# Optimization experiments

Measured on AMD Instinct MI355X. Metric: run time of the kernel, lower is better.

## Reference

```python
import jax, jax.numpy as jnp
import numpy as np

N1, N2, D = 8192, 8192, 128

def setup_inputs() -> dict:
    key = jax.random.key(0)
    k1, k2, k3, k4 = jax.random.split(key, 4)
    X1 = jax.random.normal(k1, (N1, D), dtype=jnp.float32)
    X2 = jax.random.normal(k2, (N2, D), dtype=jnp.float32)
    task1 = jax.random.randint(k3, (N1,), 0, 2, dtype=jnp.int32)
    task2 = jax.random.randint(k4, (N2,), 0, 2, dtype=jnp.int32)
    # learned parameters (init values match module defaults: lengthscale=1, output_variance=1, b=0)
    log_l = jnp.zeros((D,), dtype=jnp.float32)          # log(1)
    log_theta_l = jnp.zeros((1,), dtype=jnp.float32)    # log(1)
    b = jnp.zeros((1,), dtype=jnp.float32)
    return {"X1": X1, "X2": X2, "log_l": log_l, "log_theta_l": log_theta_l,
            "b": b, "task1": task1, "task2": task2}

def reference(X1, X2, log_l, log_theta_l, b, task1, task2):
    l = jnp.exp(log_l)                      # (D,) ARD lengthscales
    A = X1 / l                              # (N1, D)
    B = X2 / l                              # (N2, D)
    # sum((a-b)^2) = |a|^2 + |b|^2 - 2 a.b  -> GEMM form, no (N1,N2,D) intermediate
    sq_dist = (jnp.sum(A * A, axis=1)[:, None]
               + jnp.sum(B * B, axis=1)[None, :]
               - 2.0 * (A @ B.T))
    sq_dist = jnp.maximum(sq_dist, 0.0)
    K_base = jnp.exp(log_theta_l[0]) * jnp.exp(-0.5 * sq_dist)   # (N1, N2)
    # lambda = clip(2/(1+exp(b)) - 1, 0, 1)
    lam = jnp.clip(2.0 / (1.0 + jnp.exp(b[0])) - 1.0, 0.0, 1.0)
    diff_task = task1[:, None] != task2[None, :]                 # (N1, N2) bool
    K = K_base * jnp.where(diff_task, lam, 1.0)
    return K
```

## Files before the change

kernel.cpp:

```cpp
#include <hip/hip_runtime.h>
#include <stdint.h>

typedef float f32x4 __attribute__((ext_vector_type(4)));
typedef int   i32x4 __attribute__((ext_vector_type(4)));
typedef __bf16 bf16x8 __attribute__((ext_vector_type(8)));

#define NN 8192
#define DDIM 128

#define APRIME_OFF 0u
#define BPRIME_OFF (8192u*512u)
#define NORM_OFF   (268435456u - 65536u)

__device__ __forceinline__ uint32_t pk2(__bf16 a, __bf16 b) {
    return (uint32_t)__builtin_bit_cast(unsigned short, a)
         | ((uint32_t)__builtin_bit_cast(unsigned short, b) << 16);
}

__device__ __forceinline__ void gload_lds16(const void* g, void* l) {
    __builtin_amdgcn_global_load_lds(
        (const __attribute__((address_space(1))) uint32_t*)g,
        (__attribute__((address_space(3))) uint32_t*)l,
        16, 0, 0);
}

__global__ __launch_bounds__(256) void prep_kernel(
    const float* __restrict__ X1, const float* __restrict__ X2,
    const float* __restrict__ log_l, char* __restrict__ outbuf)
{
    int t = threadIdx.x, wave = t >> 6, lane = t & 63;
    int row = blockIdx.x * 4 + wave;
    const float* X; uint32_t base; float* nrm;
    if (row < NN) {
        X = X1 + (size_t)row * DDIM;
        base = APRIME_OFF + (uint32_t)row * 512u;
        nrm = (float*)(outbuf + NORM_OFF) + row;
    } else {
        int r2 = row - NN;
        X = X2 + (size_t)r2 * DDIM;
        base = BPRIME_OFF + (uint32_t)r2 * 512u;
        nrm = (float*)(outbuf + NORM_OFF) + NN + r2;
    }
    int c0 = lane * 2;
    float2 x = *(const float2*)(X + c0);
    float a0 = x.x * __expf(-log_l[c0]);
    float a1 = x.y * __expf(-log_l[c0 + 1]);
    float ss = a0 * a0 + a1 * a1;
    #pragma unroll
    for (int o = 32; o; o >>= 1) ss += __shfl_down(ss, o);
    if (lane == 0) *nrm = ss;
    __bf16 h0 = (__bf16)a0, h1 = (__bf16)a1;
    __bf16 l0 = (__bf16)(a0 - (float)h0), l1 = (__bf16)(a1 - (float)h1);
    int m = lane >> 2;
    int c = m >> 2;
    int sh = m & 3;
    int sl = 4 | sh;
    int rs = row & 7;
    uint32_t offh = base + (uint32_t)c * 128u + (uint32_t)((sh ^ rs) * 16) + (uint32_t)(lane & 3) * 4u;
    uint32_t offl = base + (uint32_t)c * 128u + (uint32_t)((sl ^ rs) * 16) + (uint32_t)(lane & 3) * 4u;
    *(uint32_t*)(outbuf + offh) = pk2(h0, h1);
    *(uint32_t*)(outbuf + offl) = pk2(l0, l1);
}

__global__ __launch_bounds__(256, 3) void fast_kernel(
    const char* __restrict__ stash,
    const int* __restrict__ task1, const int* __restrict__ task2,
    const float* __restrict__ log_theta_l, const float* __restrict__ bparam,
    float* __restrict__ C)
{
    __shared__ __align__(16) char smem[32768];
    const int t = threadIdx.x;
    const int lane = t & 63, wv = t >> 6;
    const int wr = wv >> 1, wc = wv & 1;
    const int lr = lane & 15, lg = lane >> 4;

    int wg = blockIdx.x;
    int swz = (wg & 7) * 488 + (wg >> 3);
    int tm = 2 + (swz >> 6);
    int tn = swz & 63;

    const char* Abase = stash + APRIME_OFF + (size_t)tm * 128 * 512;
    const char* Bbase = stash + BPRIME_OFF + (size_t)tn * 128 * 512;

    f32x4 acc[4][4];
    #pragma unroll
    for (int i = 0; i < 4; ++i)
        #pragma unroll
        for (int j = 0; j < 4; ++j) acc[i][j] = (f32x4){0.f, 0.f, 0.f, 0.f};

    #define STAGE(c) do {                                                         \
        _Pragma("unroll")                                                         \
        for (int i = 0; i < 4; ++i) {                                             \
            int l = t + i * 256;                                                  \
            gload_lds16(Abase + (size_t)(l >> 3) * 512 + (c) * 128 + (l & 7) * 16,\
                        smem + l * 16);                                           \
            gload_lds16(Bbase + (size_t)(l >> 3) * 512 + (c) * 128 + (l & 7) * 16,\
                        smem + 16384 + l * 16);                                   \
        }                                                                         \
    } while (0)

    #define FRAGMM() do {                                                         \
        bf16x8 ah[4], bh[4], xf[4];                                               \
        _Pragma("unroll")                                                         \
        for (int mi = 0; mi < 4; ++mi) {                                          \
            int row = wr * 64 + mi * 16 + lr;                                     \
            ah[mi] = *(const bf16x8*)(smem + row * 128 + ((lg ^ (row & 7)) * 16));\
        }                                                                         \
        _Pragma("unroll")                                                         \
        for (int ni = 0; ni < 4; ++ni) {                                          \
            int row = wc * 64 + ni * 16 + lr;                                     \
            bh[ni] = *(const bf16x8*)(smem + 16384 + row * 128                    \
                      + ((lg ^ (row & 7)) * 16));                                 \
        }                                                                         \
        _Pragma("unroll")                                                         \
        for (int mi = 0; mi < 4; ++mi)                                            \
            _Pragma("unroll")                                                     \
            for (int ni = 0; ni < 4; ++ni)                                        \
                acc[mi][ni] = __builtin_amdgcn_mfma_f32_16x16x32_bf16(            \
                    bh[ni], ah[mi], acc[mi][ni], 0, 0, 0);                        \
        _Pragma("unroll")                                                         \
        for (int mi = 0; mi < 4; ++mi) {                                          \
            int row = wr * 64 + mi * 16 + lr;                                     \
            xf[mi] = *(const bf16x8*)(smem + row * 128                            \
                      + (((4 | lg) ^ (row & 7)) * 16));                           \
        }                                                                         \
        _Pragma("unroll")                                                         \
        for (int mi = 0; mi < 4; ++mi)                                            \
            _Pragma("unroll")                                                     \
            for (int ni = 0; ni < 4; ++ni)                                        \
                acc[mi][ni] = __builtin_amdgcn_mfma_f32_16x16x32_bf16(            \
                    bh[ni], xf[mi], acc[mi][ni], 0, 0, 0);                        \
        _Pragma("unroll")                                                         \
        for (int ni = 0; ni < 4; ++ni) {                                          \
            int row = wc * 64 + ni * 16 + lr;                                     \
            xf[ni] = *(const bf16x8*)(smem + 16384 + row * 128                    \
                      + (((4 | lg) ^ (row & 7)) * 16));                           \
        }                                                                         \
        _Pragma("unroll")                                                         \
        for (int mi = 0; mi < 4; ++mi)                                            \
            _Pragma("unroll")                                                     \
            for (int ni = 0; ni < 4; ++ni)                                        \
                acc[mi][ni] = __builtin_amdgcn_mfma_f32_16x16x32_bf16(            \
                    xf[ni], ah[mi], acc[mi][ni], 0, 0, 0);                        \
    } while (0)

    STAGE(0);
    __syncthreads();
    FRAGMM();
    #pragma unroll
    for (int c = 1; c < 4; ++c) {
        __syncthreads();
        STAGE(c);
        __syncthreads();
        FRAGMM();
    }

    const float* n1g = (const float*)(stash + NORM_OFF);
    const float* n2g = n1g + NN;
    float logt = log_theta_l[0];
    float bb = bparam[0];
    float lam = fminf(fmaxf(2.f / (1.f + __expf(bb)) - 1.f, 0.f), 1.f);
    int rbase = tm * 128, cbase = tn * 128;

    #pragma unroll
    for (int mi = 0; mi < 4; ++mi) {
        int rowl = wr * 64 + mi * 16 + lr;
        float n1v = n1g[rbase + rowl];
        int t1v = task1[rbase + rowl];
        #pragma unroll
        for (int ni = 0; ni < 4; ++ni) {
            int coll = wc * 64 + ni * 16 + lg * 4;
            f32x4 n2v = *(const f32x4*)(n2g + cbase + coll);
            i32x4 t2v = *(const i32x4*)(task2 + cbase + coll);
            f32x4 kv;
            #pragma unroll
            for (int rix = 0; rix < 4; ++rix) {
                float s = fmaxf(n1v + n2v[rix] - 2.f * acc[mi][ni][rix], 0.f);
                float k = __expf(fmaf(-0.5f, s, logt));
                kv[rix] = (t1v != t2v[rix]) ? k * lam : k;
            }
            *(f32x4*)(C + (size_t)(rbase + rowl) * NN + cbase + coll) = kv;
        }
    }
    #undef STAGE
    #undef FRAGMM
}

#define RSTRIDE 80
#define S_AH 0
#define S_AL 10240
#define S_BH 20480
#define S_BL 30720
#define S_ILS 40960
#define S_N1  41472
#define S_N2  41984
#define S_TOT 42496

__device__ __forceinline__ void split4(f32x4 x, uint2& hi, uint2& lo) {
    __bf16 h0 = (__bf16)x[0], h1 = (__bf16)x[1], h2 = (__bf16)x[2], h3 = (__bf16)x[3];
    hi.x = pk2(h0, h1); hi.y = pk2(h2, h3);
    __bf16 l0 = (__bf16)(x[0] - (float)h0);
    __bf16 l1 = (__bf16)(x[1] - (float)h1);
    __bf16 l2 = (__bf16)(x[2] - (float)h2);
    __bf16 l3 = (__bf16)(x[3] - (float)h3);
    lo.x = pk2(l0, l1); lo.y = pk2(l2, l3);
}

__device__ __forceinline__ void lds_barrier() {
    asm volatile("s_waitcnt lgkmcnt(0)" ::: "memory");
    __builtin_amdgcn_sched_barrier(0);
    __builtin_amdgcn_s_barrier();
    __builtin_amdgcn_sched_barrier(0);
}

__global__ __launch_bounds__(256, 3) void slow_kernel(
    const float* __restrict__ X1, const float* __restrict__ X2,
    const float* __restrict__ log_l,
    const float* __restrict__ log_theta_l, const float* __restrict__ bparam,
    const int* __restrict__ task1, const int* __restrict__ task2,
    float* __restrict__ C)
{
    __shared__ __align__(16) char smem[S_TOT];
    float* const ils = (float*)(smem + S_ILS);
    float* const n1s = (float*)(smem + S_N1);
    float* const n2s = (float*)(smem + S_N2);

    const int t = threadIdx.x;
    const int lane = t & 63;
    const int wv = t >> 6;
    const int wr = wv >> 1, wc = wv & 1;
    const int lr = lane & 15, lg = lane >> 4;
    const int kq = t & 7;
    const int rg = t >> 3;

    int wg = blockIdx.x;
    int tsel = wg >> 6;
    int tm = (tsel == 2) ? 63 : tsel;
    int tn = wg & 63;

    const float* Ag = X1 + (size_t)tm * 128 * DDIM;
    const float* Bg = X2 + (size_t)tn * 128 * DDIM;

    if (t < 128) ils[t] = __expf(-log_l[t]);

    f32x4 aV[4], bV[4];
    #pragma unroll
    for (int e = 0; e < 4; ++e) {
        aV[e] = *(const f32x4*)(Ag + (size_t)(e * 32 + rg) * DDIM + kq * 4);
        bV[e] = *(const f32x4*)(Bg + (size_t)(e * 32 + rg) * DDIM + kq * 4);
    }
    __syncthreads();

    float nA[4] = {0.f, 0.f, 0.f, 0.f};
    float nB[4] = {0.f, 0.f, 0.f, 0.f};
    f32x4 acc[4][4];
    #pragma unroll
    for (int i = 0; i < 4; ++i)
        #pragma unroll
        for (int j = 0; j < 4; ++j) acc[i][j] = (f32x4){0.f, 0.f, 0.f, 0.f};

    for (int c = 0; c < 4; ++c) {
        {
            f32x4 il4 = *(const f32x4*)(ils + c * 32 + kq * 4);
            #pragma unroll
            for (int e = 0; e < 4; ++e) {
                int rr = e * 32 + rg;
                f32x4 xa = aV[e] * il4;
                f32x4 xb = bV[e] * il4;
                nA[e] += xa[0]*xa[0] + xa[1]*xa[1] + xa[2]*xa[2] + xa[3]*xa[3];
                nB[e] += xb[0]*xb[0] + xb[1]*xb[1] + xb[2]*xb[2] + xb[3]*xb[3];
                uint2 hA, lA, hB, lB;
                split4(xa, hA, lA);
                split4(xb, hB, lB);
                int boff = rr * RSTRIDE + kq * 8;
                *(uint2*)(smem + S_AH + boff) = hA;
                *(uint2*)(smem + S_AL + boff) = lA;
                *(uint2*)(smem + S_BH + boff) = hB;
                *(uint2*)(smem + S_BL + boff) = lB;
            }
        }
        if (c < 3) {
            #pragma unroll
            for (int e = 0; e < 4; ++e) {
                aV[e] = *(const f32x4*)(Ag + (size_t)(e * 32 + rg) * DDIM + (c + 1) * 32 + kq * 4);
                bV[e] = *(const f32x4*)(Bg + (size_t)(e * 32 + rg) * DDIM + (c + 1) * 32 + kq * 4);
            }
        }
        lds_barrier();
        {
            bf16x8 ah[4], bh[4], xf[4];
            #pragma unroll
            for (int mi = 0; mi < 4; ++mi) {
                int off = (wr * 64 + mi * 16 + lr) * RSTRIDE + lg * 16;
                ah[mi] = *(const bf16x8*)(smem + S_AH + off);
            }
            #pragma unroll
            for (int ni = 0; ni < 4; ++ni) {
                int off = (wc * 64 + ni * 16 + lr) * RSTRIDE + lg * 16;
                bh[ni] = *(const bf16x8*)(smem + S_BH + off);
            }
            #pragma unroll
            for (int mi = 0; mi < 4; ++mi)
                #pragma unroll
                for (int ni = 0; ni < 4; ++ni)
                    acc[mi][ni] = __builtin_amdgcn_mfma_f32_16x16x32_bf16(bh[ni], ah[mi], acc[mi][ni], 0, 0, 0);
            #pragma unroll
            for (int mi = 0; mi < 4; ++mi) {
                int off = (wr * 64 + mi * 16 + lr) * RSTRIDE + lg * 16;
                xf[mi] = *(const bf16x8*)(smem + S_AL + off);
            }
            #pragma unroll
            for (int mi = 0; mi < 4; ++mi)
                #pragma unroll
                for (int ni = 0; ni < 4; ++ni)
                    acc[mi][ni] = __builtin_amdgcn_mfma_f32_16x16x32_bf16(bh[ni], xf[mi], acc[mi][ni], 0, 0, 0);
            #pragma unroll
            for (int ni = 0; ni < 4; ++ni) {
                int off = (wc * 64 + ni * 16 + lr) * RSTRIDE + lg * 16;
                xf[ni] = *(const bf16x8*)(smem + S_BL + off);
            }
            #pragma unroll
            for (int mi = 0; mi < 4; ++mi)
                #pragma unroll
                for (int ni = 0; ni < 4; ++ni)
                    acc[mi][ni] = __builtin_amdgcn_mfma_f32_16x16x32_bf16(xf[ni], ah[mi], acc[mi][ni], 0, 0, 0);
        }
        lds_barrier();
    }

    #pragma unroll
    for (int e = 0; e < 4; ++e) {
        #pragma unroll
        for (int off = 1; off < 8; off <<= 1) {
            nA[e] += __shfl_xor(nA[e], off);
            nB[e] += __shfl_xor(nB[e], off);
        }
    }
    if (kq == 0) {
        #pragma unroll
        for (int e = 0; e < 4; ++e) {
            n1s[e * 32 + rg] = nA[e];
            n2s[e * 32 + rg] = nB[e];
        }
    }
    __syncthreads();

    float logt = log_theta_l[0];
    float bb = bparam[0];
    float lam = fminf(fmaxf(2.f / (1.f + __expf(bb)) - 1.f, 0.f), 1.f);
    int rbase = tm * 128, cbase = tn * 128;

    #pragma unroll
    for (int mi = 0; mi < 4; ++mi) {
        int rowl = wr * 64 + mi * 16 + lr;
        float n1v = n1s[rowl];
        int t1v = task1[rbase + rowl];
        #pragma unroll
        for (int ni = 0; ni < 4; ++ni) {
            int coll = wc * 64 + ni * 16 + lg * 4;
            f32x4 n2v = *(const f32x4*)(n2s + coll);
            i32x4 t2v = *(const i32x4*)(task2 + cbase + coll);
            f32x4 kv;
            #pragma unroll
            for (int rix = 0; rix < 4; ++rix) {
                float s = fmaxf(n1v + n2v[rix] - 2.f * acc[mi][ni][rix], 0.f);
                float k = __expf(fmaf(-0.5f, s, logt));
                kv[rix] = (t1v != t2v[rix]) ? k * lam : k;
            }
            *(f32x4*)(C + (size_t)(rbase + rowl) * NN + cbase + coll) = kv;
        }
    }
}

extern "C" void kernel_launch(void* const* d_in, const int* in_sizes, int n_in,
                              void* d_out, int out_size, void* d_ws, size_t ws_size,
                              hipStream_t stream)
{
    const float* X1 = (const float*)d_in[0];
    const float* X2 = (const float*)d_in[1];
    const float* log_l = (const float*)d_in[2];
    const float* log_theta = (const float*)d_in[3];
    const float* bp = (const float*)d_in[4];
    const int* t1 = (const int*)d_in[5];
    const int* t2 = (const int*)d_in[6];
    float* C = (float*)d_out;
    (void)d_ws; (void)ws_size; (void)in_sizes; (void)n_in; (void)out_size;

    prep_kernel<<<4096, 256, 0, stream>>>(X1, X2, log_l, (char*)d_out);
    fast_kernel<<<3904, 256, 0, stream>>>((const char*)d_out, t1, t2, log_theta, bp, C);
    slow_kernel<<<192, 256, 0, stream>>>(X1, X2, log_l, log_theta, bp, t1, t2, C);
}
```

Baseline: 101.0 us.

## Split tail tile rows and slow-kernel tiles into 64x64 quarter blocks

The fast kernel now handles tile row 62 as 256 quarter-sized 64x64 blocks instead of full 128x128 tiles, and the slow kernel (rows 0, 1, 63, whose stash region overlaps the output) is split into 768 quarter-tile blocks instead of 192 full tiles. The goal is better load balance and more parallelism in the tail of each launch, so the small slow kernel is not bound by a handful of long-running workgroups. In exchange, the quarter tiles reuse less data per load and pay more per-block overhead.

```diff
diff --git a/kernel.cpp b/kernel.cpp
--- a/kernel.cpp
+++ b/kernel.cpp
@@ -71,130 +71,235 @@
     __shared__ __align__(16) char smem[32768];
     const int t = threadIdx.x;
     const int lane = t & 63, wv = t >> 6;
-    const int wr = wv >> 1, wc = wv & 1;
     const int lr = lane & 15, lg = lane >> 4;
-
-    int wg = blockIdx.x;
-    int swz = (wg & 7) * 488 + (wg >> 3);
-    int tm = 2 + (swz >> 6);
-    int tn = swz & 63;
-
-    const char* Abase = stash + APRIME_OFF + (size_t)tm * 128 * 512;
-    const char* Bbase = stash + BPRIME_OFF + (size_t)tn * 128 * 512;
-
-    f32x4 acc[4][4];
-    #pragma unroll
-    for (int i = 0; i < 4; ++i)
-        #pragma unroll
-        for (int j = 0; j < 4; ++j) acc[i][j] = (f32x4){0.f, 0.f, 0.f, 0.f};
-
-    #define STAGE(c) do {                                                         \
-        _Pragma("unroll")                                                         \
-        for (int i = 0; i < 4; ++i) {                                             \
-            int l = t + i * 256;                                                  \
-            gload_lds16(Abase + (size_t)(l >> 3) * 512 + (c) * 128 + (l & 7) * 16,\
-                        smem + l * 16);                                           \
-            gload_lds16(Bbase + (size_t)(l >> 3) * 512 + (c) * 128 + (l & 7) * 16,\
-                        smem + 16384 + l * 16);                                   \
-        }                                                                         \
-    } while (0)
-
-    #define FRAGMM() do {                                                         \
-        bf16x8 ah[4], bh[4], xf[4];                                               \
-        _Pragma("unroll")                                                         \
-        for (int mi = 0; mi < 4; ++mi) {                                          \
-            int row = wr * 64 + mi * 16 + lr;                                     \
-            ah[mi] = *(const bf16x8*)(smem + row * 128 + ((lg ^ (row & 7)) * 16));\
-        }                                                                         \
-        _Pragma("unroll")                                                         \
-        for (int ni = 0; ni < 4; ++ni) {                                          \
-            int row = wc * 64 + ni * 16 + lr;                                     \
-            bh[ni] = *(const bf16x8*)(smem + 16384 + row * 128                    \
-                      + ((lg ^ (row & 7)) * 16));                                 \
-        }                                                                         \
-        _Pragma("unroll")                                                         \
-        for (int mi = 0; mi < 4; ++mi)                                            \
-            _Pragma("unroll")                                                     \
-            for (int ni = 0; ni < 4; ++ni)                                        \
-                acc[mi][ni] = __builtin_amdgcn_mfma_f32_16x16x32_bf16(            \
-                    bh[ni], ah[mi], acc[mi][ni], 0, 0, 0);                        \
-        _Pragma("unroll")                                                         \
-        for (int mi = 0; mi < 4; ++mi) {                                          \
-            int row = wr * 64 + mi * 16 + lr;                                     \
-            xf[mi] = *(const bf16x8*)(smem + row * 128                            \
-                      + (((4 | lg) ^ (row & 7)) * 16));                           \
-        }                                                                         \
-        _Pragma("unroll")                                                         \
-        for (int mi = 0; mi < 4; ++mi)                                            \
-            _Pragma("unroll")                                                     \
-            for (int ni = 0; ni < 4; ++ni)                                        \
-                acc[mi][ni] = __builtin_amdgcn_mfma_f32_16x16x32_bf16(            \
-                    bh[ni], xf[mi], acc[mi][ni], 0, 0, 0);                        \
-        _Pragma("unroll")                                                         \
-        for (int ni = 0; ni < 4; ++ni) {                                          \
-            int row = wc * 64 + ni * 16 + lr;                                     \
-            xf[ni] = *(const bf16x8*)(smem + 16384 + row * 128                    \
-                      + (((4 | lg) ^ (row & 7)) * 16));                           \
-        }                                                                         \
-        _Pragma("unroll")                                                         \
-        for (int mi = 0; mi < 4; ++mi)                                            \
-            _Pragma("unroll")                                                     \
-            for (int ni = 0; ni < 4; ++ni)                                        \
-                acc[mi][ni] = __builtin_amdgcn_mfma_f32_16x16x32_bf16(            \
-                    xf[ni], ah[mi], acc[mi][ni], 0, 0, 0);                        \
-    } while (0)
-
-    STAGE(0);
-    __syncthreads();
-    FRAGMM();
-    #pragma unroll
-    for (int c = 1; c < 4; ++c) {
-        __syncthreads();
-        STAGE(c);
-        __syncthreads();
-        FRAGMM();
-    }
-
     const float* n1g = (const float*)(stash + NORM_OFF);
     const float* n2g = n1g + NN;
     float logt = log_theta_l[0];
     float bb = bparam[0];
     float lam = fminf(fmaxf(2.f / (1.f + __expf(bb)) - 1.f, 0.f), 1.f);
-    int rbase = tm * 128, cbase = tn * 128;
-
-    #pragma unroll
-    for (int mi = 0; mi < 4; ++mi) {
-        int rowl = wr * 64 + mi * 16 + lr;
-        float n1v = n1g[rbase + rowl];
-        int t1v = task1[rbase + rowl];
-        #pragma unroll
-        for (int ni = 0; ni < 4; ++ni) {
-            int coll = wc * 64 + ni * 16 + lg * 4;
-            f32x4 n2v = *(const f32x4*)(n2g + cbase + coll);
-            i32x4 t2v = *(const i32x4*)(task2 + cbase + coll);
-            f32x4 kv;
-            #pragma unroll
-            for (int rix = 0; rix < 4; ++rix) {
-                float s = fmaxf(n1v + n2v[rix] - 2.f * acc[mi][ni][rix], 0.f);
-                float k = __expf(fmaf(-0.5f, s, logt));
-                kv[rix] = (t1v != t2v[rix]) ? k * lam : k;
-            }
-            *(f32x4*)(C + (size_t)(rbase + rowl) * NN + cbase + coll) = kv;
-        }
-    }
-    #undef STAGE
-    #undef FRAGMM
+    int wg = blockIdx.x;
+
+    if (wg < 3840) {
+        const int wr = wv >> 1, wc = wv & 1;
+        int swz = (wg & 7) * 480 + (wg >> 3);
+        int tm = 2 + (swz >> 6);
+        int tn = swz & 63;
+        const char* Abase = stash + APRIME_OFF + (size_t)tm * 128 * 512;
+        const char* Bbase = stash + BPRIME_OFF + (size_t)tn * 128 * 512;
+
+        f32x4 acc[4][4];
+        #pragma unroll
+        for (int i = 0; i < 4; ++i)
+            #pragma unroll
+            for (int j = 0; j < 4; ++j) acc[i][j] = (f32x4){0.f, 0.f, 0.f, 0.f};
+
+        #define STAGE_F(c) do {                                                       \
+            _Pragma("unroll")                                                         \
+            for (int i = 0; i < 4; ++i) {                                             \
+                int l = t + i * 256;                                                  \
+                gload_lds16(Abase + (size_t)(l >> 3) * 512 + (c) * 128 + (l & 7) * 16,\
+                            smem + l * 16);                                           \
+                gload_lds16(Bbase + (size_t)(l >> 3) * 512 + (c) * 128 + (l & 7) * 16,\
+                            smem + 16384 + l * 16);                                   \
+            }                                                                         \
+        } while (0)
+
+        #define FRAGMM_F() do {                                                       \
+            bf16x8 ah[4], bh[4], xf[4];                                               \
+            _Pragma("unroll")                                                         \
+            for (int mi = 0; mi < 4; ++mi) {                                          \
+                int row = wr * 64 + mi * 16 + lr;                                     \
+                ah[mi] = *(const bf16x8*)(smem + row * 128 + ((lg ^ (row & 7)) * 16));\
+            }                                                                         \
+            _Pragma("unroll")                                                         \
+            for (int ni = 0; ni < 4; ++ni) {                                          \
+                int row = wc * 64 + ni * 16 + lr;                                     \
+                bh[ni] = *(const bf16x8*)(smem + 16384 + row * 128                    \
+                          + ((lg ^ (row & 7)) * 16));                                 \
+            }                                                                         \
+            _Pragma("unroll")                                                         \
+            for (int mi = 0; mi < 4; ++mi)                                            \
+                _Pragma("unroll")                                                     \
+                for (int ni = 0; ni < 4; ++ni)                                        \
+                    acc[mi][ni] = __builtin_amdgcn_mfma_f32_16x16x32_bf16(            \
+                        bh[ni], ah[mi], acc[mi][ni], 0, 0, 0);                        \
+            _Pragma("unroll")                                                         \
+            for (int mi = 0; mi < 4; ++mi) {                                          \
+                int row = wr * 64 + mi * 16 + lr;                                     \
+                xf[mi] = *(const bf16x8*)(smem + row * 128                            \
+                          + (((4 | lg) ^ (row & 7)) * 16));                           \
+            }                                                                         \
+            _Pragma("unroll")                                                         \
+            for (int mi = 0; mi < 4; ++mi)                                            \
+                _Pragma("unroll")                                                     \
+                for (int ni = 0; ni < 4; ++ni)                                        \
+                    acc[mi][ni] = __builtin_amdgcn_mfma_f32_16x16x32_bf16(            \
+                        bh[ni], xf[mi], acc[mi][ni], 0, 0, 0);                        \
+            _Pragma("unroll")                                                         \
+            for (int ni = 0; ni < 4; ++ni) {                                          \
+                int row = wc * 64 + ni * 16 + lr;                                     \
+                xf[ni] = *(const bf16x8*)(smem + 16384 + row * 128                    \
+                          + (((4 | lg) ^ (row & 7)) * 16));                           \
+            }                                                                         \
+            _Pragma("unroll")                                                         \
+            for (int mi = 0; mi < 4; ++mi)                                            \
+                _Pragma("unroll")                                                     \
+                for (int ni = 0; ni < 4; ++ni)                                        \
+                    acc[mi][ni] = __builtin_amdgcn_mfma_f32_16x16x32_bf16(            \
+                        xf[ni], ah[mi], acc[mi][ni], 0, 0, 0);                        \
+        } while (0)
+
+        STAGE_F(0);
+        __syncthreads();
+        FRAGMM_F();
+        #pragma unroll
+        for (int c = 1; c < 4; ++c) {
+            __syncthreads();
+            STAGE_F(c);
+            __syncthreads();
+            FRAGMM_F();
+        }
+
+        int rbase = tm * 128, cbase = tn * 128;
+        #pragma unroll
+        for (int mi = 0; mi < 4; ++mi) {
+            int rowl = wr * 64 + mi * 16 + lr;
+            float n1v = n1g[rbase + rowl];
+            int t1v = task1[rbase + rowl];
+            #pragma unroll
+            for (int ni = 0; ni < 4; ++ni) {
+                int coll = wc * 64 + ni * 16 + lg * 4;
+                f32x4 n2v = *(const f32x4*)(n2g + cbase + coll);
+                i32x4 t2v = *(const i32x4*)(task2 + cbase + coll);
+                f32x4 kv;
+                #pragma unroll
+                for (int rix = 0; rix < 4; ++rix) {
+                    float s = fmaxf(n1v + n2v[rix] - 2.f * acc[mi][ni][rix], 0.f);
+                    float k = __expf(fmaf(-0.5f, s, logt));
+                    kv[rix] = (t1v != t2v[rix]) ? k * lam : k;
+                }
+                *(f32x4*)(C + (size_t)(rbase + rowl) * NN + cbase + coll) = kv;
+            }
+        }
+        #undef STAGE_F
+        #undef FRAGMM_F
+    } else {
+        int wq = wg - 3840;
+        int tn = wq >> 2;
+        int q = wq & 3;
+        int arow0 = 62 * 128 + (q >> 1) * 64;
+        int brow0 = tn * 128 + (q & 1) * 64;
+        const int wr = wv >> 1, wc = wv & 1;
+        const char* Abase = stash + APRIME_OFF + (size_t)arow0 * 512;
+        const char* Bbase = stash + BPRIME_OFF + (size_t)brow0 * 512;
+
+        f32x4 acc[2][2];
+        #pragma unroll
+        for (int i = 0; i < 2; ++i)
+            #pragma unroll
+            for (int j = 0; j < 2; ++j) acc[i][j] = (f32x4){0.f, 0.f, 0.f, 0.f};
+
+        #define STAGE_Q(c) do {                                                       \
+            _Pragma("unroll")                                                         \
+            for (int i = 0; i < 2; ++i) {                                             \
+                int l = t + i * 256;                                                  \
+                gload_lds16(Abase + (size_t)(l >> 3) * 512 + (c) * 128 + (l & 7) * 16,\
+                            smem + l * 16);                                           \
+                gload_lds16(Bbase + (size_t)(l >> 3) * 512 + (c) * 128 + (l & 7) * 16,\
+                            smem + 8192 + l * 16);                                    \
+            }                                                                         \
+        } while (0)
+
+        #define FRAGMM_Q() do {                                                       \
+            bf16x8 ah[2], bh[2], xf[2];                                               \
+            _Pragma("unroll")                                                         \
+            for (int mi = 0; mi < 2; ++mi) {                                          \
+                int row = wr * 32 + mi * 16 + lr;                                     \
+                ah[mi] = *(const bf16x8*)(smem + row * 128 + ((lg ^ (row & 7)) * 16));\
+            }                                                                         \
+            _Pragma("unroll")                                                         \
+            for (int ni = 0; ni < 2; ++ni) {                                          \
+                int row = wc * 32 + ni * 16 + lr;                                     \
+                bh[ni] = *(const bf16x8*)(smem + 8192 + row * 128                     \
+                          + ((lg ^ (row & 7)) * 16));                                 \
+            }                                                                         \
+            _Pragma("unroll")                                                         \
+            for (int mi = 0; mi < 2; ++mi)                                            \
+                _Pragma("unroll")                                                     \
+                for (int ni = 0; ni < 2; ++ni)                                        \
+                    acc[mi][ni] = __builtin_amdgcn_mfma_f32_16x16x32_bf16(            \
+                        bh[ni], ah[mi], acc[mi][ni], 0, 0, 0);                        \
+            _Pragma("unroll")                                                         \
+            for (int mi = 0; mi < 2; ++mi) {                                          \
+                int row = wr * 32 + mi * 16 + lr;                                     \
+                xf[mi] = *(const bf16x8*)(smem + row * 128                            \
+                          + (((4 | lg) ^ (row & 7)) * 16));                           \
+            }                                                                         \
+            _Pragma("unroll")                                                         \
+            for (int mi = 0; mi < 2; ++mi)                                            \
+                _Pragma("unroll")                                                     \
+                for (int ni = 0; ni < 2; ++ni)                                        \
+                    acc[mi][ni] = __builtin_amdgcn_mfma_f32_16x16x32_bf16(            \
+                        bh[ni], xf[mi], acc[mi][ni], 0, 0, 0);                        \
+            _Pragma("unroll")                                                         \
+            for (int ni = 0; ni < 2; ++ni) {                                          \
+                int row = wc * 32 + ni * 16 + lr;                                     \
+                xf[ni] = *(const bf16x8*)(smem + 8192 + row * 128                     \
+                          + (((4 | lg) ^ (row & 7)) * 16));                           \
+            }                                                                         \
+            _Pragma("unroll")                                                         \
+            for (int mi = 0; mi < 2; ++mi)                                            \
+                _Pragma("unroll")                                                     \
+                for (int ni = 0; ni < 2; ++ni)                                        \
+                    acc[mi][ni] = __builtin_amdgcn_mfma_f32_16x16x32_bf16(            \
+                        xf[ni], ah[mi], acc[mi][ni], 0, 0, 0);                        \
+        } while (0)
+
+        STAGE_Q(0);
+        __syncthreads();
+        FRAGMM_Q();
+        #pragma unroll
+        for (int c = 1; c < 4; ++c) {
+            __syncthreads();
+            STAGE_Q(c);
+            __syncthreads();
+            FRAGMM_Q();
+        }
+
+        #pragma unroll
+        for (int mi = 0; mi < 2; ++mi) {
+            int rowl = wr * 32 + mi * 16 + lr;
+            float n1v = n1g[arow0 + rowl];
+            int t1v = task1[arow0 + rowl];
+            #pragma unroll
+            for (int ni = 0; ni < 2; ++ni) {
+                int coll = wc * 32 + ni * 16 + lg * 4;
+                f32x4 n2v = *(const f32x4*)(n2g + brow0 + coll);
+                i32x4 t2v = *(const i32x4*)(task2 + brow0 + coll);
+                f32x4 kv;
+                #pragma unroll
+                for (int rix = 0; rix < 4; ++rix) {
+                    float s = fmaxf(n1v + n2v[rix] - 2.f * acc[mi][ni][rix], 0.f);
+                    float k = __expf(fmaf(-0.5f, s, logt));
+                    kv[rix] = (t1v != t2v[rix]) ? k * lam : k;
+                }
+                *(f32x4*)(C + (size_t)(arow0 + rowl) * NN + brow0 + coll) = kv;
+            }
+        }
+        #undef STAGE_Q
+        #undef FRAGMM_Q
+    }
 }
 
 #define RSTRIDE 80
-#define S_AH 0
-#define S_AL 10240
-#define S_BH 20480
-#define S_BL 30720
-#define S_ILS 40960
-#define S_N1  41472
-#define S_N2  41984
-#define S_TOT 42496
+#define SQ_AH 0
+#define SQ_AL 5120
+#define SQ_BH 10240
+#define SQ_BL 15360
+#define SQ_ILS 20480
+#define SQ_N1  20992
+#define SQ_N2  21504
+#define SQ_TOT 22016
 
 __device__ __forceinline__ void split4(f32x4 x, uint2& hi, uint2& lo) {
     __bf16 h0 = (__bf16)x[0], h1 = (__bf16)x[1], h2 = (__bf16)x[2], h3 = (__bf16)x[3];
@@ -220,10 +325,10 @@
     const int* __restrict__ task1, const int* __restrict__ task2,
     float* __restrict__ C)
 {
-    __shared__ __align__(16) char smem[S_TOT];
-    float* const ils = (float*)(smem + S_ILS);
-    float* const n1s = (float*)(smem + S_N1);
-    float* const n2s = (float*)(smem + S_N2);
+    __shared__ __align__(16) char smem[SQ_TOT];
+    float* const ils = (float*)(smem + SQ_ILS);
+    float* const n1s = (float*)(smem + SQ_N1);
+    float* const n2s = (float*)(smem + SQ_N2);
 
     const int t = threadIdx.x;
     const int lane = t & 63;
@@ -234,36 +339,40 @@
     const int rg = t >> 3;
 
     int wg = blockIdx.x;
-    int tsel = wg >> 6;
+    int ti = wg >> 2;
+    int tsel = ti >> 6;
     int tm = (tsel == 2) ? 63 : tsel;
-    int tn = wg & 63;
-
-    const float* Ag = X1 + (size_t)tm * 128 * DDIM;
-    const float* Bg = X2 + (size_t)tn * 128 * DDIM;
+    int tn = ti & 63;
+    int q = wg & 3;
+    int row0 = tm * 128 + (q >> 1) * 64;
+    int col0 = tn * 128 + (q & 1) * 64;
+
+    const float* Ag = X1 + (size_t)row0 * DDIM;
+    const float* Bg = X2 + (size_t)col0 * DDIM;
 
     if (t < 128) ils[t] = __expf(-log_l[t]);
 
-    f32x4 aV[4], bV[4];
+    f32x4 aV[2], bV[2];
     #pragma unroll
-    for (int e = 0; e < 4; ++e) {
+    for (int e = 0; e < 2; ++e) {
         aV[e] = *(const f32x4*)(Ag + (size_t)(e * 32 + rg) * DDIM + kq * 4);
         bV[e] = *(const f32x4*)(Bg + (size_t)(e * 32 + rg) * DDIM + kq * 4);
     }
     __syncthreads();
 
-    float nA[4] = {0.f, 0.f, 0.f, 0.f};
-    float nB[4] = {0.f, 0.f, 0.f, 0.f};
-    f32x4 acc[4][4];
+    float nA[2] = {0.f, 0.f};
+    float nB[2] = {0.f, 0.f};
+    f32x4 acc[2][2];
     #pragma unroll
-    for (int i = 0; i < 4; ++i)
-        #pragma unroll
-        for (int j = 0; j < 4; ++j) acc[i][j] = (f32x4){0.f, 0.f, 0.f, 0.f};
+    for (int i = 0; i < 2; ++i)
+        #pragma unroll
+        for (int j = 0; j < 2; ++j) acc[i][j] = (f32x4){0.f, 0.f, 0.f, 0.f};
 
     for (int c = 0; c < 4; ++c) {
         {
             f32x4 il4 = *(const f32x4*)(ils + c * 32 + kq * 4);
             #pragma unroll
-            for (int e = 0; e < 4; ++e) {
+            for (int e = 0; e < 2; ++e) {
                 int rr = e * 32 + rg;
                 f32x4 xa = aV[e] * il4;
                 f32x4 xb = bV[e] * il4;
@@ -273,63 +382,63 @@
                 split4(xa, hA, lA);
                 split4(xb, hB, lB);
                 int boff = rr * RSTRIDE + kq * 8;
-                *(uint2*)(smem + S_AH + boff) = hA;
-                *(uint2*)(smem + S_AL + boff) = lA;
-                *(uint2*)(smem + S_BH + boff) = hB;
-                *(uint2*)(smem + S_BL + boff) = lB;
+                *(uint2*)(smem + SQ_AH + boff) = hA;
+                *(uint2*)(smem + SQ_AL + boff) = lA;
+                *(uint2*)(smem + SQ_BH + boff) = hB;
+                *(uint2*)(smem + SQ_BL + boff) = lB;
             }
         }
         if (c < 3) {
             #pragma unroll
-            for (int e = 0; e < 4; ++e) {
+            for (int e = 0; e < 2; ++e) {
                 aV[e] = *(const f32x4*)(Ag + (size_t)(e * 32 + rg) * DDIM + (c + 1) * 32 + kq * 4);
                 bV[e] = *(const f32x4*)(Bg + (size_t)(e * 32 + rg) * DDIM + (c + 1) * 32 + kq * 4);
             }
         }
         lds_barrier();
         {
-            bf16x8 ah[4], bh[4], xf[4];
-            #pragma unroll
-            for (int mi = 0; mi < 4; ++mi) {
-                int off = (wr * 64 + mi * 16 + lr) * RSTRIDE + lg * 16;
-                ah[mi] = *(const bf16x8*)(smem + S_AH + off);
-            }
-            #pragma unroll
-            for (int ni = 0; ni < 4; ++ni) {
-                int off = (wc * 64 + ni * 16 + lr) * RSTRIDE + lg * 16;
-                bh[ni] = *(const bf16x8*)(smem + S_BH + off);
-            }
-            #pragma unroll
-            for (int mi = 0; mi < 4; ++mi)
+            bf16x8 ah[2], bh[2], xf[2];
+            #pragma unroll
+            for (int mi = 0; mi < 2; ++mi) {
+                int off = (wr * 32 + mi * 16 + lr) * RSTRIDE + lg * 16;
+                ah[mi] = *(const bf16x8*)(smem + SQ_AH + off);
+            }
+            #pragma unroll
+            for (int ni = 0; ni < 2; ++ni) {
+                int off = (wc * 32 + ni * 16 + lr) * RSTRIDE + lg * 16;
+                bh[ni] = *(const bf16x8*)(smem + SQ_BH + off);
+            }
+            #pragma unroll
+            for (int mi = 0; mi < 2; ++mi)
                 #pragma unroll
-                for (int ni = 0; ni < 4; ++ni)
+                for (int ni = 0; ni < 2; ++ni)
                     acc[mi][ni] = __builtin_amdgcn_mfma_f32_16x16x32_bf16(bh[ni], ah[mi], acc[mi][ni], 0, 0, 0);
             #pragma unroll
-            for (int mi = 0; mi < 4; ++mi) {
-                int off = (wr * 64 + mi * 16 + lr) * RSTRIDE + lg * 16;
-                xf[mi] = *(const bf16x8*)(smem + S_AL + off);
-            }
-            #pragma unroll
-            for (int mi = 0; mi < 4; ++mi)
+            for (int mi = 0; mi < 2; ++mi) {
+                int off = (wr * 32 + mi * 16 + lr) * RSTRIDE + lg * 16;
+                xf[mi] = *(const bf16x8*)(smem + SQ_AL + off);
+            }
+            #pragma unroll
+            for (int mi = 0; mi < 2; ++mi)
                 #pragma unroll
-                for (int ni = 0; ni < 4; ++ni)
+                for (int ni = 0; ni < 2; ++ni)
                     acc[mi][ni] = __builtin_amdgcn_mfma_f32_16x16x32_bf16(bh[ni], xf[mi], acc[mi][ni], 0, 0, 0);
             #pragma unroll
-            for (int ni = 0; ni < 4; ++ni) {
-                int off = (wc * 64 + ni * 16 + lr) * RSTRIDE + lg * 16;
-                xf[ni] = *(const bf16x8*)(smem + S_BL + off);
-            }
-            #pragma unroll
-            for (int mi = 0; mi < 4; ++mi)
+            for (int ni = 0; ni < 2; ++ni) {
+                int off = (wc * 32 + ni * 16 + lr) * RSTRIDE + lg * 16;
+                xf[ni] = *(const bf16x8*)(smem + SQ_BL + off);
+            }
+            #pragma unroll
+            for (int mi = 0; mi < 2; ++mi)
                 #pragma unroll
-                for (int ni = 0; ni < 4; ++ni)
+                for (int ni = 0; ni < 2; ++ni)
                     acc[mi][ni] = __builtin_amdgcn_mfma_f32_16x16x32_bf16(xf[ni], ah[mi], acc[mi][ni], 0, 0, 0);
         }
         lds_barrier();
     }
 
     #pragma unroll
-    for (int e = 0; e < 4; ++e) {
+    for (int e = 0; e < 2; ++e) {
         #pragma unroll
         for (int off = 1; off < 8; off <<= 1) {
             nA[e] += __shfl_xor(nA[e], off);
@@ -338,7 +447,7 @@
     }
     if (kq == 0) {
         #pragma unroll
-        for (int e = 0; e < 4; ++e) {
+        for (int e = 0; e < 2; ++e) {
             n1s[e * 32 + rg] = nA[e];
             n2s[e * 32 + rg] = nB[e];
         }
@@ -348,18 +457,17 @@
     float logt = log_theta_l[0];
     float bb = bparam[0];
     float lam = fminf(fmaxf(2.f / (1.f + __expf(bb)) - 1.f, 0.f), 1.f);
-    int rbase = tm * 128, cbase = tn * 128;
 
     #pragma unroll
-    for (int mi = 0; mi < 4; ++mi) {
-        int rowl = wr * 64 + mi * 16 + lr;
+    for (int mi = 0; mi < 2; ++mi) {
+        int rowl = wr * 32 + mi * 16 + lr;
         float n1v = n1s[rowl];
-        int t1v = task1[rbase + rowl];
-        #pragma unroll
-        for (int ni = 0; ni < 4; ++ni) {
-            int coll = wc * 64 + ni * 16 + lg * 4;
+        int t1v = task1[row0 + rowl];
+        #pragma unroll
+        for (int ni = 0; ni < 2; ++ni) {
+            int coll = wc * 32 + ni * 16 + lg * 4;
             f32x4 n2v = *(const f32x4*)(n2s + coll);
-            i32x4 t2v = *(const i32x4*)(task2 + cbase + coll);
+            i32x4 t2v = *(const i32x4*)(task2 + col0 + coll);
             f32x4 kv;
             #pragma unroll
             for (int rix = 0; rix < 4; ++rix) {
@@ -367,7 +475,7 @@
                 float k = __expf(fmaf(-0.5f, s, logt));
                 kv[rix] = (t1v != t2v[rix]) ? k * lam : k;
             }
-            *(f32x4*)(C + (size_t)(rbase + rowl) * NN + cbase + coll) = kv;
+            *(f32x4*)(C + (size_t)(row0 + rowl) * NN + col0 + coll) = kv;
         }
     }
 }
@@ -387,6 +495,6 @@
     (void)d_ws; (void)ws_size; (void)in_sizes; (void)n_in; (void)out_size;
 
     prep_kernel<<<4096, 256, 0, stream>>>(X1, X2, log_l, (char*)d_out);
-    fast_kernel<<<3904, 256, 0, stream>>>((const char*)d_out, t1, t2, log_theta, bp, C);
-    slow_kernel<<<192, 256, 0, stream>>>(X1, X2, log_l, log_theta, bp, t1, t2, C);
-}
+    fast_kernel<<<4096, 256, 0, stream>>>((const char*)d_out, t1, t2, log_theta, bp, C);
+    slow_kernel<<<768, 256, 0, stream>>>(X1, X2, log_l, log_theta, bp, t1, t2, C);
+}
```

New measurement: 97.95 us. -3.0%, faster.
